# Kernel optimization log

Measured on AMD Instinct MI355X. Metric: run time of the kernel, lower is better.

The kernel has to match this reference:

```python
import jax, jax.numpy as jnp
from jax import lax
import numpy as np

D_STATE = 16
D_CONV = 4
GROUPS = 4
TOKEN = 8


def group_norm(x, w, b, groups, eps=1e-5):
    # x: [B, C, H, W]; torch GroupNorm semantics
    B, C, H, W = x.shape
    xg = x.reshape(B, groups, C // groups, H, W)
    mu = xg.mean(axis=(2, 3, 4), keepdims=True)
    var = ((xg - mu) ** 2).mean(axis=(2, 3, 4), keepdims=True)
    xg = (xg - mu) / jnp.sqrt(var + eps)
    return xg.reshape(B, C, H, W) * w[None, :, None, None] + b[None, :, None, None]


def mamba_fwd(x, in_w, conv_w, conv_b, xproj_w, dt_w, dt_b, A_log, D, out_w):
    # x: [B, L, d_model]. Faithful mamba_ssm Mamba forward (no biases on in/out proj).
    Bsz, L, _ = x.shape
    d_inner = in_w.shape[0] // 2
    dt_rank = dt_w.shape[1]
    xz = x @ in_w.T                                   # [B, L, 2*d_inner]
    xi, z = jnp.split(xz, 2, axis=-1)
    # causal depthwise conv1d (kernel D_CONV) + SiLU
    xc = lax.conv_general_dilated(
        xi.transpose(0, 2, 1), conv_w, window_strides=(1,),
        padding=[(D_CONV - 1, 0)], dimension_numbers=("NCH", "OIH", "NCH"),
        feature_group_count=d_inner)
    xc = jax.nn.silu(xc + conv_b[None, :, None]).transpose(0, 2, 1)  # [B, L, d_inner]
    xdb = xc @ xproj_w.T                               # [B, L, dt_rank + 2*d_state]
    dt, Bm, Cm = jnp.split(xdb, [dt_rank, dt_rank + D_STATE], axis=-1)
    dt = jax.nn.softplus(dt @ dt_w.T + dt_b)           # [B, L, d_inner]
    A = -jnp.exp(A_log)                                # [d_inner, d_state]
    dA = jnp.exp(dt[..., None] * A)                    # [B, L, d_inner, d_state]
    dBx = dt[..., None] * Bm[:, :, None, :] * xc[..., None]

    def step(h, inp):
        dA_t, dBx_t, C_t = inp                         # [B,di,ds],[B,di,ds],[B,ds]
        h = dA_t * h + dBx_t
        y = jnp.einsum('bds,bs->bd', h, C_t)
        return h, y

    h0 = jnp.zeros((Bsz, d_inner, D_STATE), dtype=x.dtype)
    _, ys = lax.scan(step, h0, (dA.transpose(1, 0, 2, 3),
                                dBx.transpose(1, 0, 2, 3),
                                Cm.transpose(1, 0, 2)))
    y = ys.transpose(1, 0, 2) + xc * D                 # skip term D*x
    y = y * jax.nn.silu(z)
    return y @ out_w.T


def setup_inputs() -> dict:
    key = jax.random.key(0)
    ks = iter(jax.random.split(key, 48))

    def rn(shape, s=0.02):
        return jax.random.normal(next(ks), shape, dtype=jnp.float32) * s

    B, C, H, W = 4, 64, 64, 64
    inp = {"x": jax.random.normal(next(ks), (B, C, H, W), dtype=jnp.float32)}

    def mamba_params(prefix, d_model):
        d_inner = 2 * d_model
        dt_rank = -(-d_model // 16)
        inp[prefix + "_in_w"] = rn((2 * d_inner, d_model))
        inp[prefix + "_conv_w"] = rn((d_inner, 1, D_CONV))
        inp[prefix + "_conv_b"] = rn((d_inner,))
        inp[prefix + "_xproj_w"] = rn((dt_rank + 2 * D_STATE, d_inner))
        inp[prefix + "_dt_w"] = rn((d_inner, dt_rank))
        inp[prefix + "_dt_b"] = rn((d_inner,)) + 0.5
        inp[prefix + "_A_log"] = jnp.log(jnp.tile(jnp.arange(1, D_STATE + 1, dtype=jnp.float32), (d_inner, 1)))
        inp[prefix + "_D"] = jnp.ones((d_inner,), jnp.float32)
        inp[prefix + "_out_w"] = rn((d_model, d_inner))

    mamba_params("spa", C)
    mamba_params("spe", -(-C // TOKEN))  # group_channel_num = ceil(64/8) = 8
    inp["spa_gn_w"] = jnp.ones((C,), jnp.float32)
    inp["spa_gn_b"] = jnp.zeros((C,), jnp.float32)
    inp["spe_gn_w"] = jnp.ones((C,), jnp.float32)
    inp["spe_gn_b"] = jnp.zeros((C,), jnp.float32)
    inp["att_w"] = jnp.full((2,), 0.5, jnp.float32)
    return inp


def reference(x,
              spa_in_w, spa_conv_w, spa_conv_b, spa_xproj_w, spa_dt_w, spa_dt_b,
              spa_A_log, spa_D, spa_out_w,
              spe_in_w, spe_conv_w, spe_conv_b, spe_xproj_w, spe_dt_w, spe_dt_b,
              spe_A_log, spe_D, spe_out_w,
              spa_gn_w, spa_gn_b, spe_gn_w, spe_gn_b, att_w):
    B, C, H, W = x.shape
    gcn = -(-C // TOKEN)  # C == TOKEN*gcn here, so no padding path is taken

    # --- SpaMamba: flatten all pixels into one sequence [1, B*H*W, C] ---
    xs = x.transpose(0, 2, 3, 1).reshape(1, -1, C)
    ys = mamba_fwd(xs, spa_in_w, spa_conv_w, spa_conv_b, spa_xproj_w,
                   spa_dt_w, spa_dt_b, spa_A_log, spa_D, spa_out_w)
    ys = ys.reshape(B, H, W, C).transpose(0, 3, 1, 2)
    spa = jax.nn.silu(group_norm(ys, spa_gn_w, spa_gn_b, GROUPS)) + x

    # --- SpeMamba: per-pixel spectral tokens [B*H*W, TOKEN, gcn] ---
    xe = x.transpose(0, 2, 3, 1).reshape(B * H * W, TOKEN, gcn)
    ye = mamba_fwd(xe, spe_in_w, spe_conv_w, spe_conv_b, spe_xproj_w,
                   spe_dt_w, spe_dt_b, spe_A_log, spe_D, spe_out_w)
    ye = ye.reshape(B, H, W, C).transpose(0, 3, 1, 2)
    spe = x + jax.nn.silu(group_norm(ye, spe_gn_w, spe_gn_b, GROUPS))

    w = jax.nn.softmax(att_w)
    return spa * w[0] + spe * w[1] + x
```

## Files before the change

kernel.cpp:

```cpp
#include <hip/hip_runtime.h>

__device__ __forceinline__ float siluf(float x){ return x / (1.f + __expf(-x)); }
__device__ __forceinline__ float softplusf(float x){
    return fmaxf(x, 0.f) + __logf(1.f + __expf(-fabsf(x)));
}
#if __has_builtin(__builtin_amdgcn_exp2f)
__device__ __forceinline__ float fexp2(float x){ return __builtin_amdgcn_exp2f(x); }
#else
__device__ __forceinline__ float fexp2(float x){ return exp2f(x); }
#endif

__global__ void __launch_bounds__(256) k_xpose(const float* __restrict__ x, float* __restrict__ xs){
    __shared__ float t[64][65];
    int blk = blockIdx.x;
    int b = blk >> 6;
    int hw0 = (blk & 63) << 6;
    int tid = threadIdx.x;
    if (blk == 0 && tid < 192) xs[tid] = 0.f;
    const float* xb = x + b*262144 + hw0;
    #pragma unroll
    for (int it = 0; it < 16; ++it){
        int idx = it*256 + tid;
        t[idx>>6][idx&63] = xb[(idx>>6)*4096 + (idx&63)];
    }
    __syncthreads();
    float* xsb = xs + 192 + (size_t)(b*4096 + hw0)*64;
    #pragma unroll
    for (int it = 0; it < 16; ++it){
        int idx = it*256 + tid;
        xsb[(idx>>6)*64 + (idx&63)] = t[idx&63][idx>>6];
    }
}

__global__ void __launch_bounds__(256) k_inproj_conv(const float* __restrict__ xs,
        const float* __restrict__ in_w, const float* __restrict__ cw, const float* __restrict__ cb,
        float* __restrict__ xc, float* __restrict__ zb){
    int tid = threadIdx.x;
    int l0 = blockIdx.x * 8;
    float wr[64];
    const float4* w4 = (const float4*)(in_w + tid*64);
    #pragma unroll
    for (int k = 0; k < 16; ++k){
        float4 v = w4[k];
        wr[4*k]=v.x; wr[4*k+1]=v.y; wr[4*k+2]=v.z; wr[4*k+3]=v.w;
    }
    if (tid < 128){
        float acc[11];
        #pragma unroll
        for (int r = 0; r < 11; ++r) acc[r] = 0.f;
        const float4* xr = ((const float4*)xs) + (size_t)l0*16;
        #pragma unroll
        for (int k = 0; k < 16; ++k){
            #pragma unroll
            for (int r = 0; r < 11; ++r){
                float4 v = xr[r*16 + k];
                acc[r] = fmaf(v.x, wr[4*k],   acc[r]);
                acc[r] = fmaf(v.y, wr[4*k+1], acc[r]);
                acc[r] = fmaf(v.z, wr[4*k+2], acc[r]);
                acc[r] = fmaf(v.w, wr[4*k+3], acc[r]);
            }
        }
        float cw0 = cw[tid*4+0], cw1 = cw[tid*4+1], cw2 = cw[tid*4+2], cw3 = cw[tid*4+3];
        float cbd = cb[tid];
        #pragma unroll
        for (int r = 0; r < 8; ++r){
            float a = fmaf(cw0, acc[r],   cbd);
            a = fmaf(cw1, acc[r+1], a);
            a = fmaf(cw2, acc[r+2], a);
            a = fmaf(cw3, acc[r+3], a);
            xc[(size_t)(l0+r)*128 + tid] = siluf(a);
        }
    } else {
        float acc[8];
        #pragma unroll
        for (int r = 0; r < 8; ++r) acc[r] = 0.f;
        const float4* xr = ((const float4*)(xs + 192)) + (size_t)l0*16;
        #pragma unroll
        for (int k = 0; k < 16; ++k){
            #pragma unroll
            for (int r = 0; r < 8; ++r){
                float4 v = xr[r*16 + k];
                acc[r] = fmaf(v.x, wr[4*k],   acc[r]);
                acc[r] = fmaf(v.y, wr[4*k+1], acc[r]);
                acc[r] = fmaf(v.z, wr[4*k+2], acc[r]);
                acc[r] = fmaf(v.w, wr[4*k+3], acc[r]);
            }
        }
        int dz = tid - 128;
        #pragma unroll
        for (int r = 0; r < 8; ++r) zb[(size_t)(l0+r)*128 + dz] = acc[r];
    }
}

__global__ void __launch_bounds__(256) k_scan_p1(const float* __restrict__ xc,
        const float* __restrict__ xpw, const float* __restrict__ dtw, const float* __restrict__ dtb,
        const float* __restrict__ A_log, float* __restrict__ Pb, float* __restrict__ Qb){
    __shared__ float sxc[2048];
    __shared__ float sbm[256];
    __shared__ __align__(16) float dtr[64];
    const int tid = threadIdx.x;
    const int ch = blockIdx.x;
    {
        const float4* src = (const float4*)(xc + (size_t)ch*2048);
        float4* dst = (float4*)sxc;
        dst[tid] = src[tid];
        dst[256 + tid] = src[256 + tid];
    }
    __syncthreads();
    {
        int j = tid & 63, tg = tid >> 6;
        if (j < 20){
            const float4* w4  = (const float4*)(xpw + j*128);
            const float4* xc4 = (const float4*)sxc + tg*128;
            float acc[4];
            #pragma unroll
            for (int r = 0; r < 4; ++r) acc[r] = 0.f;
            #pragma unroll 8
            for (int k = 0; k < 32; ++k){
                float4 w = w4[k];
                #pragma unroll
                for (int r = 0; r < 4; ++r){
                    float4 v = xc4[r*32 + k];
                    acc[r] = fmaf(v.x, w.x, acc[r]);
                    acc[r] = fmaf(v.y, w.y, acc[r]);
                    acc[r] = fmaf(v.z, w.z, acc[r]);
                    acc[r] = fmaf(v.w, w.w, acc[r]);
                }
            }
            if (j < 4){
                #pragma unroll
                for (int r = 0; r < 4; ++r) dtr[(tg*4+r)*4 + j] = acc[r];
            } else {
                #pragma unroll
                for (int r = 0; r < 4; ++r) sbm[(tg*4+r)*16 + (j-4)] = acc[r];
            }
        }
    }
    __syncthreads();
    const int d  = tid & 127;
    const int sh = tid >> 7;
    float A8[8];
    {
        const float4* al4 = (const float4*)(A_log + d*16 + sh*8);
        float4 v0 = al4[0], v1 = al4[1];
        A8[0]=-__expf(v0.x)*1.44269504f; A8[1]=-__expf(v0.y)*1.44269504f;
        A8[2]=-__expf(v0.z)*1.44269504f; A8[3]=-__expf(v0.w)*1.44269504f;
        A8[4]=-__expf(v1.x)*1.44269504f; A8[5]=-__expf(v1.y)*1.44269504f;
        A8[6]=-__expf(v1.z)*1.44269504f; A8[7]=-__expf(v1.w)*1.44269504f;
    }
    float4 dw = *(const float4*)(dtw + d*4);
    float dbd = dtb[d];
    float P[8], Q[8];
    #pragma unroll
    for (int s = 0; s < 8; ++s){ P[s] = 1.f; Q[s] = 0.f; }
    #pragma unroll 4
    for (int i = 0; i < 16; ++i){
        float4 dt4 = *(const float4*)(dtr + i*4);
        float dv = dbd;
        dv = fmaf(dt4.x, dw.x, dv);
        dv = fmaf(dt4.y, dw.y, dv);
        dv = fmaf(dt4.z, dw.z, dv);
        dv = fmaf(dt4.w, dw.w, dv);
        float dt = softplusf(dv);
        float db = dt * sxc[i*128 + d];
        const float4* bmr = (const float4*)(sbm + i*16 + sh*8);
        float4 b0 = bmr[0], b1 = bmr[1];
        float bv[8] = {b0.x,b0.y,b0.z,b0.w,b1.x,b1.y,b1.z,b1.w};
        #pragma unroll
        for (int s = 0; s < 8; ++s){
            float a = fexp2(dt*A8[s]);
            P[s] *= a;
            Q[s] = fmaf(a, Q[s], db*bv[s]);
        }
    }
    float* Pp = Pb + (size_t)ch*2048 + d*16 + sh*8;
    float* Qp = Qb + (size_t)ch*2048 + d*16 + sh*8;
    ((float4*)Pp)[0] = make_float4(P[0],P[1],P[2],P[3]);
    ((float4*)Pp)[1] = make_float4(P[4],P[5],P[6],P[7]);
    ((float4*)Qp)[0] = make_float4(Q[0],Q[1],Q[2],Q[3]);
    ((float4*)Qp)[1] = make_float4(Q[4],Q[5],Q[6],Q[7]);
}

#define XE_  0
#define XCL_ 1216
#define BCL_ 3904
#define DTV_ 8640
#define SPG_ 8768
__global__ void __launch_bounds__(256) k_spe(
        const float* __restrict__ x,
        const float* __restrict__ ein_w, const float* __restrict__ ecw, const float* __restrict__ ecb,
        const float* __restrict__ expw, const float* __restrict__ edtw, const float* __restrict__ edtb,
        const float* __restrict__ eA_log, const float* __restrict__ eDv, const float* __restrict__ eow,
        float* __restrict__ ye, float* __restrict__ sp)
{
    __shared__ float smem[8800];
    const int tid = threadIdx.x;
    const int pix = tid >> 4;
    const int d   = tid & 15;
    const int eb  = blockIdx.x;
    const int p0  = eb * 16;
    const int b   = p0 >> 12;
    const int hw0 = p0 & 4095;

    const float* xb = x + b*262144 + hw0;
    #pragma unroll
    for (int it = 0; it < 4; ++it){
        int idx = it*256 + tid;
        smem[XE_ + (idx&15)*76 + (idx>>4)] = xb[(idx>>4)*4096 + (idx&15)];
    }
    __syncthreads();

    float wi[8], wz[8];
    #pragma unroll
    for (int g = 0; g < 8; ++g){ wi[g] = ein_w[d*8+g]; wz[g] = ein_w[(16+d)*8+g]; }
    float xi[8], zz[8];
    {
        const float4* xe4 = (const float4*)(smem + XE_ + pix*76);
        #pragma unroll
        for (int t = 0; t < 8; ++t){
            float4 a = xe4[t*2], bq = xe4[t*2+1];
            float xv8[8] = {a.x,a.y,a.z,a.w,bq.x,bq.y,bq.z,bq.w};
            float ai = 0.f, az = 0.f;
            #pragma unroll
            for (int g = 0; g < 8; ++g){
                ai = fmaf(xv8[g], wi[g], ai);
                az = fmaf(xv8[g], wz[g], az);
            }
            xi[t] = ai; zz[t] = az;
        }
    }
    float c0 = ecw[d*4+0], c1 = ecw[d*4+1], c2 = ecw[d*4+2], c3 = ecw[d*4+3];
    float cbd = ecb[d];
    float xcr[8];
    #pragma unroll
    for (int t = 0; t < 8; ++t){
        float a = fmaf(c3, xi[t], cbd);
        if (t >= 1) a = fmaf(c2, xi[t-1], a);
        if (t >= 2) a = fmaf(c1, xi[t-2], a);
        if (t >= 3) a = fmaf(c0, xi[t-3], a);
        xcr[t] = siluf(a);
        smem[XCL_ + pix*168 + t*20 + d] = xcr[t];
    }
    __syncthreads();

    {
        const int row = tid & 127;
        const int jh  = tid >> 7;
        const int px2 = row >> 3;
        const int t2  = row & 7;
        const float4* xr = (const float4*)(smem + XCL_ + px2*168 + t2*20);
        float4 r0 = xr[0], r1 = xr[1], r2 = xr[2], r3 = xr[3];
        float xv[16] = {r0.x,r0.y,r0.z,r0.w, r1.x,r1.y,r1.z,r1.w,
                        r2.x,r2.y,r2.z,r2.w, r3.x,r3.y,r3.z,r3.w};
        const float* wbase = expw + (1 + jh*16)*16;
        float outv[16];
        #pragma unroll
        for (int s = 0; s < 16; ++s){
            const float* wr = wbase + s*16;
            float a = 0.f;
            #pragma unroll
            for (int k = 0; k < 16; ++k) a = fmaf(xv[k], wr[k], a);
            outv[s] = a;
        }
        float4* dst4 = (float4*)(smem + BCL_ + px2*296 + t2*36 + jh*16);
        dst4[0] = make_float4(outv[0], outv[1], outv[2], outv[3]);
        dst4[1] = make_float4(outv[4], outv[5], outv[6], outv[7]);
        dst4[2] = make_float4(outv[8], outv[9], outv[10],outv[11]);
        dst4[3] = make_float4(outv[12],outv[13],outv[14],outv[15]);
        if (jh == 0){
            float accd = 0.f;
            #pragma unroll
            for (int k = 0; k < 16; ++k) accd = fmaf(xv[k], expw[k], accd);
            smem[DTV_ + px2*8 + t2] = accd;
        }
    }
    __syncthreads();

    float A16[16];
    #pragma unroll
    for (int s = 0; s < 16; ++s) A16[s] = -__expf(eA_log[d*16+s]) * 1.44269504f;
    float dwd = edtw[d], dbd = edtb[d], Dd = eDv[d];
    float h[16];
    #pragma unroll
    for (int s = 0; s < 16; ++s) h[s] = 0.f;
    #pragma unroll
    for (int t = 0; t < 8; ++t){
        float dtd = softplusf(fmaf(smem[DTV_ + pix*8 + t], dwd, dbd));
        float db = dtd * xcr[t];
        const float4* bc4 = (const float4*)(smem + BCL_ + pix*296 + t*36);
        float4 b0 = bc4[0], b1 = bc4[1], b2 = bc4[2], b3 = bc4[3];
        float4 cc0 = bc4[4], cc1 = bc4[5], cc2 = bc4[6], cc3 = bc4[7];
        float bv[16] = {b0.x,b0.y,b0.z,b0.w, b1.x,b1.y,b1.z,b1.w,
                        b2.x,b2.y,b2.z,b2.w, b3.x,b3.y,b3.z,b3.w};
        float cv[16] = {cc0.x,cc0.y,cc0.z,cc0.w, cc1.x,cc1.y,cc1.z,cc1.w,
                        cc2.x,cc2.y,cc2.z,cc2.w, cc3.x,cc3.y,cc3.z,cc3.w};
        float yp = 0.f;
        #pragma unroll
        for (int s = 0; s < 16; ++s){
            float a = fexp2(dtd*A16[s]);
            h[s] = fmaf(a, h[s], db*bv[s]);
            yp = fmaf(h[s], cv[s], yp);
        }
        smem[pix*168 + t*20 + d] = (yp + xcr[t]*Dd) * siluf(zz[t]);
    }
    __syncthreads();

    {
        const int half = tid >> 7;
        const int idx7 = tid & 127;
        const int pixD = idx7 >> 3;
        const int ttD  = idx7 & 7;
        const int m0   = half*4;
        const float4* y4 = (const float4*)(smem + pixD*168 + ttD*20);
        float4 y0 = y4[0], y1 = y4[1], y2 = y4[2], y3 = y4[3];
        float ylr[16] = {y0.x,y0.y,y0.z,y0.w, y1.x,y1.y,y1.z,y1.w,
                         y2.x,y2.y,y2.z,y2.w, y3.x,y3.y,y3.z,y3.w};
        float acc[4];
        #pragma unroll
        for (int mm = 0; mm < 4; ++mm){
            const float* wr = eow + (m0+mm)*16;
            float a = 0.f;
            #pragma unroll
            for (int k = 0; k < 16; ++k) a = fmaf(ylr[k], wr[k], a);
            acc[mm] = a;
        }
        float4 o; o.x=acc[0]; o.y=acc[1]; o.z=acc[2]; o.w=acc[3];
        *(float4*)(ye + (size_t)(p0+pixD)*64 + ttD*8 + m0) = o;

        float s  = acc[0]+acc[1]+acc[2]+acc[3];
        float ss = acc[0]*acc[0]+acc[1]*acc[1]+acc[2]*acc[2]+acc[3]*acc[3];
        s += __shfl_xor(s,1);  ss += __shfl_xor(ss,1);
        s += __shfl_xor(s,8);  ss += __shfl_xor(ss,8);
        s += __shfl_xor(s,16); ss += __shfl_xor(ss,16);
        s += __shfl_xor(s,32); ss += __shfl_xor(ss,32);
        int lane = tid & 63, wv = tid >> 6;
        if ((lane & 57) == 0){
            smem[SPG_ + wv*4 + ((lane>>1)&3)] = s;
            smem[SPG_ + 16 + wv*4 + ((lane>>1)&3)] = ss;
        }
    }
    __syncthreads();
    if (tid < 4){
        int blk = eb & 255;
        float S  = smem[SPG_+0*4+tid]+smem[SPG_+1*4+tid]+smem[SPG_+2*4+tid]+smem[SPG_+3*4+tid];
        float SS = smem[SPG_+16+0*4+tid]+smem[SPG_+16+1*4+tid]+smem[SPG_+16+2*4+tid]+smem[SPG_+16+3*4+tid];
        float* dst = sp + (size_t)(((4 + b)*4 + tid)*512 + blk*2);
        dst[0] = S; dst[1] = SS;
    }
}

__global__ void __launch_bounds__(256) k_scan_p2a(const float* __restrict__ Pb,
        const float* __restrict__ Qb, float* __restrict__ Ps, float* __restrict__ Qs){
    int g = blockIdx.x*256 + threadIdx.x;
    int sup = g >> 11;
    int lane = g & 2047;
    float P = 1.f, Q = 0.f;
    for (int i = 0; i < 64; i += 8){
        float p[8], q[8];
        #pragma unroll
        for (int u = 0; u < 8; ++u){
            p[u] = Pb[(size_t)(sup*64+i+u)*2048 + lane];
            q[u] = Qb[(size_t)(sup*64+i+u)*2048 + lane];
        }
        #pragma unroll
        for (int u = 0; u < 8; ++u){
            P = p[u]*P;
            Q = fmaf(p[u], Q, q[u]);
        }
    }
    Ps[g] = P; Qs[g] = Q;
}

__global__ void __launch_bounds__(256) k_scan_p2c(const float* __restrict__ Pb,
        const float* __restrict__ Qb, const float* __restrict__ Ps,
        const float* __restrict__ Qs, float* __restrict__ Hs){
    int g = blockIdx.x*256 + threadIdx.x;
    int sup = g >> 11;
    int lane = g & 2047;
    float h = 0.f;
    for (int u = 0; u < sup; ++u){
        float p = Ps[u*2048 + lane];
        float q = Qs[u*2048 + lane];
        h = fmaf(p, h, q);
    }
    for (int i = 0; i < 64; i += 8){
        float p[8], q[8];
        #pragma unroll
        for (int u = 0; u < 8; ++u){
            p[u] = Pb[(size_t)(sup*64+i+u)*2048 + lane];
            q[u] = Qb[(size_t)(sup*64+i+u)*2048 + lane];
        }
        #pragma unroll
        for (int u = 0; u < 8; ++u){
            Hs[(size_t)(sup*64+i+u)*2048 + lane] = h;
            h = fmaf(p[u], h, q[u]);
        }
    }
}

__global__ void __launch_bounds__(256) k_scan_p3(const float* __restrict__ xc,
        const float* __restrict__ zb, const float* __restrict__ xpw, const float* __restrict__ dtw,
        const float* __restrict__ dtb, const float* __restrict__ A_log, const float* __restrict__ Dv,
        const float* __restrict__ Hs, const float* __restrict__ ow,
        float* __restrict__ ys, float* __restrict__ sp){
    __shared__ float sxc[16*128];
    __shared__ float ypl[2][16*128];
    __shared__ float sbm[16*16];
    __shared__ float scm[16*16];
    __shared__ __align__(16) float dtr[16][4];
    __shared__ float pgs[2][2][4];
    const int tid = threadIdx.x;
    const int ch = blockIdx.x;
    {
        const float4* src = (const float4*)(xc + (size_t)ch*2048);
        float4* dst = (float4*)sxc;
        dst[tid] = src[tid];
        dst[256 + tid] = src[256 + tid];
    }
    __syncthreads();
    {
        int j = tid & 63, tg = tid >> 6;
        if (j < 36){
            const float4* w4  = (const float4*)(xpw + j*128);
            const float4* xc4 = (const float4*)sxc + tg*128;
            float acc[4];
            #pragma unroll
            for (int r = 0; r < 4; ++r) acc[r] = 0.f;
            #pragma unroll 8
            for (int k = 0; k < 32; ++k){
                float4 w = w4[k];
                #pragma unroll
                for (int r = 0; r < 4; ++r){
                    float4 v = xc4[r*32 + k];
                    acc[r] = fmaf(v.x, w.x, acc[r]);
                    acc[r] = fmaf(v.y, w.y, acc[r]);
                    acc[r] = fmaf(v.z, w.z, acc[r]);
                    acc[r] = fmaf(v.w, w.w, acc[r]);
                }
            }
            if (j < 4){
                #pragma unroll
                for (int r = 0; r < 4; ++r) dtr[tg*4+r][j] = acc[r];
            } else if (j < 20){
                #pragma unroll
                for (int r = 0; r < 4; ++r) sbm[(tg*4+r)*16 + (j-4)] = acc[r];
            } else {
                #pragma unroll
                for (int r = 0; r < 4; ++r) scm[(tg*4+r)*16 + (j-20)] = acc[r];
            }
        }
    }
    __syncthreads();
    const int d  = tid & 127;
    const int sh = tid >> 7;
    float A8[8], h[8];
    {
        const float4* al4 = (const float4*)(A_log + d*16 + sh*8);
        float4 v0 = al4[0], v1 = al4[1];
        A8[0]=-__expf(v0.x)*1.44269504f; A8[1]=-__expf(v0.y)*1.44269504f;
        A8[2]=-__expf(v0.z)*1.44269504f; A8[3]=-__expf(v0.w)*1.44269504f;
        A8[4]=-__expf(v1.x)*1.44269504f; A8[5]=-__expf(v1.y)*1.44269504f;
        A8[6]=-__expf(v1.z)*1.44269504f; A8[7]=-__expf(v1.w)*1.44269504f;
        const float4* h4 = (const float4*)(Hs + (size_t)ch*2048 + d*16 + sh*8);
        float4 h0 = h4[0], h1 = h4[1];
        h[0]=h0.x; h[1]=h0.y; h[2]=h0.z; h[3]=h0.w;
        h[4]=h1.x; h[5]=h1.y; h[6]=h1.z; h[7]=h1.w;
    }
    float4 dw = *(const float4*)(dtw + d*4);
    float dbd = dtb[d];
    #pragma unroll 4
    for (int i = 0; i < 16; ++i){
        float4 dt4 = *(const float4*)dtr[i];
        float dv = dbd;
        dv = fmaf(dt4.x, dw.x, dv);
        dv = fmaf(dt4.y, dw.y, dv);
        dv = fmaf(dt4.z, dw.z, dv);
        dv = fmaf(dt4.w, dw.w, dv);
        float dt = softplusf(dv);
        float db = dt * sxc[i*128 + d];
        const float4* bmr = (const float4*)(sbm + i*16 + sh*8);
        const float4* cmr = (const float4*)(scm + i*16 + sh*8);
        float4 b0 = bmr[0], b1 = bmr[1];
        float4 c0 = cmr[0], c1 = cmr[1];
        float bv[8] = {b0.x,b0.y,b0.z,b0.w,b1.x,b1.y,b1.z,b1.w};
        float cv[8] = {c0.x,c0.y,c0.z,c0.w,c1.x,c1.y,c1.z,c1.w};
        float yp = 0.f;
        #pragma unroll
        for (int s = 0; s < 8; ++s){
            float a = fexp2(dt*A8[s]);
            h[s] = fmaf(a, h[s], db*bv[s]);
            yp = fmaf(h[s], cv[s], yp);
        }
        ypl[sh][i*128 + d] = yp;
    }
    __syncthreads();
    #pragma unroll
    for (int it = 0; it < 8; ++it){
        int idx = it*256 + tid;
        float yp = ypl[0][idx] + ypl[1][idx];
        float xcd = sxc[idx];
        float zv = zb[(size_t)ch*2048 + idx];
        ypl[0][idx] = (yp + xcd*Dv[idx & 127]) * siluf(zv);
    }
    __syncthreads();
    {
        int c  = tid & 63;
        int kh = (tid >> 6) & 1;
        int rg = tid >> 7;
        float wr[64];
        const float4* w4o = (const float4*)(ow + c*128 + kh*64);
        #pragma unroll
        for (int k = 0; k < 16; ++k){
            float4 v = w4o[k];
            wr[4*k]=v.x; wr[4*k+1]=v.y; wr[4*k+2]=v.z; wr[4*k+3]=v.w;
        }
        float acc[8];
        #pragma unroll
        for (int r = 0; r < 8; ++r) acc[r] = 0.f;
        const float4* y4 = (const float4*)(ypl[0] + rg*8*128 + kh*64);
        #pragma unroll
        for (int k = 0; k < 16; ++k){
            #pragma unroll
            for (int r = 0; r < 8; ++r){
                float4 v = y4[r*32 + k];
                acc[r] = fmaf(v.x, wr[4*k],   acc[r]);
                acc[r] = fmaf(v.y, wr[4*k+1], acc[r]);
                acc[r] = fmaf(v.z, wr[4*k+2], acc[r]);
                acc[r] = fmaf(v.w, wr[4*k+3], acc[r]);
            }
        }
        float* part = ypl[1];
        if (kh == 1){
            #pragma unroll
            for (int r = 0; r < 8; ++r) part[(rg*8+r)*64 + c] = acc[r];
        }
        __syncthreads();
        if (kh == 0){
            float s = 0.f, ss = 0.f;
            #pragma unroll
            for (int r = 0; r < 8; ++r){
                float v = acc[r] + part[(rg*8+r)*64 + c];
                ys[(size_t)(ch*16 + rg*8 + r)*64 + c] = v;
                s += v; ss += v*v;
            }
            s += __shfl_xor(s,1); ss += __shfl_xor(ss,1);
            s += __shfl_xor(s,2); ss += __shfl_xor(ss,2);
            s += __shfl_xor(s,4); ss += __shfl_xor(ss,4);
            s += __shfl_xor(s,8); ss += __shfl_xor(ss,8);
            if ((c & 15) == 0){ pgs[0][rg][c>>4] = s; pgs[1][rg][c>>4] = ss; }
        }
        __syncthreads();
        if (tid < 4){
            int b = ch >> 8, blk = ch & 255;
            float S  = pgs[0][0][tid] + pgs[0][1][tid];
            float SS = pgs[1][0][tid] + pgs[1][1][tid];
            float* dst = sp + (size_t)((b*4 + tid)*512 + blk*2);
            dst[0] = S; dst[1] = SS;
        }
    }
}

__global__ void __launch_bounds__(256) k_final(const float* __restrict__ x,
        const float* __restrict__ ys, const float* __restrict__ ye,
        const float* __restrict__ sp,
        const float* __restrict__ gsw, const float* __restrict__ gsb,
        const float* __restrict__ gew, const float* __restrict__ geb,
        const float* __restrict__ attw, float* __restrict__ out){
    __shared__ float st[16];
    __shared__ float tys[32][65];
    __shared__ float tye[32][65];
    int tid = threadIdx.x;
    int b   = blockIdx.x >> 7;
    int hw0 = (blockIdx.x & 127) << 5;
    {
        int combo = tid >> 5;
        int j = tid & 31;
        int t = combo >> 2, g = combo & 3;
        const float4* bp = (const float4*)(sp + (size_t)(t*16 + b*4 + g)*512 + j*16);
        float s = 0.f, ss = 0.f;
        #pragma unroll
        for (int k = 0; k < 4; ++k){ float4 v = bp[k]; s += v.x+v.z; ss += v.y+v.w; }
        s += __shfl_xor(s,1);  ss += __shfl_xor(ss,1);
        s += __shfl_xor(s,2);  ss += __shfl_xor(ss,2);
        s += __shfl_xor(s,4);  ss += __shfl_xor(ss,4);
        s += __shfl_xor(s,8);  ss += __shfl_xor(ss,8);
        s += __shfl_xor(s,16); ss += __shfl_xor(ss,16);
        if (j == 0){
            float m = s * (1.f/65536.f);
            float v = ss * (1.f/65536.f) - m*m;
            st[combo*2]   = m;
            st[combo*2+1] = rsqrtf(v + 1e-5f);
        }
    }
    const float* ysb = ys + ((size_t)(b*4096 + hw0))*64;
    const float* yeb = ye + ((size_t)(b*4096 + hw0))*64;
    #pragma unroll
    for (int it = 0; it < 8; ++it){
        int idx = it*256 + tid;
        tys[idx>>6][idx&63] = ysb[idx];
        tye[idx>>6][idx&63] = yeb[idx];
    }
    __syncthreads();
    float a0 = attw[0], a1 = attw[1];
    float mx = fmaxf(a0, a1);
    float e0 = __expf(a0-mx), e1 = __expf(a1-mx);
    float inv = 1.f/(e0+e1);
    float w0 = e0*inv, w1 = e1*inv;
    #pragma unroll
    for (int it = 0; it < 8; ++it){
        int idx = it*256 + tid;
        int c = idx >> 5, hwi = idx & 31;
        int g = c >> 4;
        size_t gx = ((size_t)(b*64 + c))*4096 + hw0 + hwi;
        float xv = x[gx];
        float ns = (tys[hwi][c] - st[g*2])     * st[g*2+1]     * gsw[c] + gsb[c];
        float ne = (tye[hwi][c] - st[8+g*2])   * st[8+g*2+1]   * gew[c] + geb[c];
        out[gx] = w0*(siluf(ns)+xv) + w1*(xv+siluf(ne)) + xv;
    }
}

#define OFF_XS 0u
#define OFF_XC 1048832u
#define OFF_Z  3145984u
#define OFF_PB 5243136u
#define OFF_QB 7340288u
#define OFF_HS 9437440u
#define OFF_YE 11534592u
#define OFF_PS 12583168u
#define OFF_QS 12615936u
#define OFF_SP 12648704u

extern "C" void kernel_launch(void* const* d_in, const int* in_sizes, int n_in,
                              void* d_out, int out_size, void* d_ws, size_t ws_size,
                              hipStream_t stream) {
    const float* x           = (const float*)d_in[0];
    const float* spa_in_w    = (const float*)d_in[1];
    const float* spa_conv_w  = (const float*)d_in[2];
    const float* spa_conv_b  = (const float*)d_in[3];
    const float* spa_xproj_w = (const float*)d_in[4];
    const float* spa_dt_w    = (const float*)d_in[5];
    const float* spa_dt_b    = (const float*)d_in[6];
    const float* spa_A_log   = (const float*)d_in[7];
    const float* spa_D       = (const float*)d_in[8];
    const float* spa_out_w   = (const float*)d_in[9];
    const float* spe_in_w    = (const float*)d_in[10];
    const float* spe_conv_w  = (const float*)d_in[11];
    const float* spe_conv_b  = (const float*)d_in[12];
    const float* spe_xproj_w = (const float*)d_in[13];
    const float* spe_dt_w    = (const float*)d_in[14];
    const float* spe_dt_b    = (const float*)d_in[15];
    const float* spe_A_log   = (const float*)d_in[16];
    const float* spe_D       = (const float*)d_in[17];
    const float* spe_out_w   = (const float*)d_in[18];
    const float* spa_gn_w    = (const float*)d_in[19];
    const float* spa_gn_b    = (const float*)d_in[20];
    const float* spe_gn_w    = (const float*)d_in[21];
    const float* spe_gn_b    = (const float*)d_in[22];
    const float* att_w       = (const float*)d_in[23];

    float* ws  = (float*)d_ws;
    float* xs  = ws + OFF_XS;
    float* xc  = ws + OFF_XC;
    float* zb  = ws + OFF_Z;
    float* Pb  = ws + OFF_PB;
    float* Qb  = ws + OFF_QB;
    float* Hs  = ws + OFF_HS;
    float* Ps  = ws + OFF_PS;
    float* Qs  = ws + OFF_QS;
    float* sp  = ws + OFF_SP;
    float* ysb = ws + OFF_XS;
    float* yeb = ws + OFF_YE;
    float* out = (float*)d_out;

    k_xpose      <<<256,  256, 0, stream>>>(x, xs);
    k_inproj_conv<<<2048, 256, 0, stream>>>(xs, spa_in_w, spa_conv_w, spa_conv_b, xc, zb);
    k_scan_p1    <<<1024, 256, 0, stream>>>(xc, spa_xproj_w, spa_dt_w, spa_dt_b, spa_A_log,
                                            Pb, Qb);
    k_spe        <<<1024, 256, 0, stream>>>(x, spe_in_w, spe_conv_w, spe_conv_b, spe_xproj_w,
                                            spe_dt_w, spe_dt_b, spe_A_log, spe_D, spe_out_w,
                                            yeb, sp);
    k_scan_p2a   <<<128,  256, 0, stream>>>(Pb, Qb, Ps, Qs);
    k_scan_p2c   <<<128,  256, 0, stream>>>(Pb, Qb, Ps, Qs, Hs);
    k_scan_p3    <<<1024, 256, 0, stream>>>(xc, zb, spa_xproj_w, spa_dt_w, spa_dt_b,
                                            spa_A_log, spa_D, Hs, spa_out_w, ysb, sp);
    k_final      <<<512,  256, 0, stream>>>(x, ysb, yeb, sp, spa_gn_w, spa_gn_b,
                                            spe_gn_w, spe_gn_b, att_w, out);
}
```

Baseline: 120.4 us.

## Fuse input transpose into in-proj kernel and stage spectral weights in LDS

Removes the separate transpose kernel. The in-projection/conv kernel now gathers its 11 channel-major rows (with a 3-row causal halo, zero-padded at the start) straight from x into shared memory, which saves one launch and a full write/read of the transposed buffer. The spectral kernel also preloads its small weight vectors into shared memory instead of reading them from global memory per thread. In exchange, the gathered reads from x are strided by 4096 floats per channel and so poorly coalesced, and the halo rows are loaded redundantly by neighbouring blocks.

```diff
diff --git a/kernel.cpp b/kernel.cpp
--- a/kernel.cpp
+++ b/kernel.cpp
@@ -10,33 +10,23 @@
 __device__ __forceinline__ float fexp2(float x){ return exp2f(x); }
 #endif
 
-__global__ void __launch_bounds__(256) k_xpose(const float* __restrict__ x, float* __restrict__ xs){
-    __shared__ float t[64][65];
-    int blk = blockIdx.x;
-    int b = blk >> 6;
-    int hw0 = (blk & 63) << 6;
-    int tid = threadIdx.x;
-    if (blk == 0 && tid < 192) xs[tid] = 0.f;
-    const float* xb = x + b*262144 + hw0;
-    #pragma unroll
-    for (int it = 0; it < 16; ++it){
-        int idx = it*256 + tid;
-        t[idx>>6][idx&63] = xb[(idx>>6)*4096 + (idx&63)];
-    }
-    __syncthreads();
-    float* xsb = xs + 192 + (size_t)(b*4096 + hw0)*64;
-    #pragma unroll
-    for (int it = 0; it < 16; ++it){
-        int idx = it*256 + tid;
-        xsb[(idx>>6)*64 + (idx&63)] = t[idx&63][idx>>6];
-    }
-}
-
-__global__ void __launch_bounds__(256) k_inproj_conv(const float* __restrict__ xs,
+__global__ void __launch_bounds__(256) k_inproj_conv(const float* __restrict__ x,
         const float* __restrict__ in_w, const float* __restrict__ cw, const float* __restrict__ cb,
         float* __restrict__ xc, float* __restrict__ zb){
+    __shared__ float sxe[11][68];
     int tid = threadIdx.x;
     int l0 = blockIdx.x * 8;
+    #pragma unroll
+    for (int it = 0; it < 3; ++it){
+        int idx = it*256 + tid;
+        if (idx < 704){
+            int r = idx >> 6, c = idx & 63;
+            int p = l0 - 3 + r;
+            float v = 0.f;
+            if (p >= 0) v = x[(size_t)(p >> 12)*262144 + c*4096 + (p & 4095)];
+            sxe[r][c] = v;
+        }
+    }
     float wr[64];
     const float4* w4 = (const float4*)(in_w + tid*64);
     #pragma unroll
@@ -44,16 +34,16 @@
         float4 v = w4[k];
         wr[4*k]=v.x; wr[4*k+1]=v.y; wr[4*k+2]=v.z; wr[4*k+3]=v.w;
     }
+    __syncthreads();
     if (tid < 128){
         float acc[11];
         #pragma unroll
         for (int r = 0; r < 11; ++r) acc[r] = 0.f;
-        const float4* xr = ((const float4*)xs) + (size_t)l0*16;
         #pragma unroll
         for (int k = 0; k < 16; ++k){
             #pragma unroll
             for (int r = 0; r < 11; ++r){
-                float4 v = xr[r*16 + k];
+                float4 v = *(const float4*)&sxe[r][4*k];
                 acc[r] = fmaf(v.x, wr[4*k],   acc[r]);
                 acc[r] = fmaf(v.y, wr[4*k+1], acc[r]);
                 acc[r] = fmaf(v.z, wr[4*k+2], acc[r]);
@@ -74,12 +64,11 @@
         float acc[8];
         #pragma unroll
         for (int r = 0; r < 8; ++r) acc[r] = 0.f;
-        const float4* xr = ((const float4*)(xs + 192)) + (size_t)l0*16;
         #pragma unroll
         for (int k = 0; k < 16; ++k){
             #pragma unroll
             for (int r = 0; r < 8; ++r){
-                float4 v = xr[r*16 + k];
+                float4 v = *(const float4*)&sxe[r+3][4*k];
                 acc[r] = fmaf(v.x, wr[4*k],   acc[r]);
                 acc[r] = fmaf(v.y, wr[4*k+1], acc[r]);
                 acc[r] = fmaf(v.z, wr[4*k+2], acc[r]);
@@ -181,11 +170,18 @@
     ((float4*)Qp)[1] = make_float4(Q[4],Q[5],Q[6],Q[7]);
 }
 
-#define XE_  0
-#define XCL_ 1216
-#define BCL_ 3904
-#define DTV_ 8640
-#define SPG_ 8768
+#define XE_   0
+#define XCL_  1216
+#define BCL_  3904
+#define DTV_  8640
+#define SPG_  8768
+#define WEIN_ 8800
+#define WECW_ 9056
+#define WECB_ 9120
+#define WEAL_ 9136
+#define WDTW_ 9392
+#define WDTB_ 9408
+#define WDV_  9424
 __global__ void __launch_bounds__(256) k_spe(
         const float* __restrict__ x,
         const float* __restrict__ ein_w, const float* __restrict__ ecw, const float* __restrict__ ecb,
@@ -193,7 +189,7 @@
         const float* __restrict__ eA_log, const float* __restrict__ eDv, const float* __restrict__ eow,
         float* __restrict__ ye, float* __restrict__ sp)
 {
-    __shared__ float smem[8800];
+    __shared__ float smem[9440];
     const int tid = threadIdx.x;
     const int pix = tid >> 4;
     const int d   = tid & 15;
@@ -202,6 +198,21 @@
     const int b   = p0 >> 12;
     const int hw0 = p0 & 4095;
 
+    #pragma unroll
+    for (int it = 0; it < 3; ++it){
+        int idx = it*256 + tid;
+        if (idx < 640){
+            float v;
+            if      (idx < 256) v = ein_w[idx];
+            else if (idx < 320) v = ecw[idx-256];
+            else if (idx < 336) v = ecb[idx-320];
+            else if (idx < 592) v = eA_log[idx-336];
+            else if (idx < 608) v = edtw[idx-592];
+            else if (idx < 624) v = edtb[idx-608];
+            else                v = eDv[idx-624];
+            smem[WEIN_ + idx] = v;
+        }
+    }
     const float* xb = x + b*262144 + hw0;
     #pragma unroll
     for (int it = 0; it < 4; ++it){
@@ -212,7 +223,7 @@
 
     float wi[8], wz[8];
     #pragma unroll
-    for (int g = 0; g < 8; ++g){ wi[g] = ein_w[d*8+g]; wz[g] = ein_w[(16+d)*8+g]; }
+    for (int g = 0; g < 8; ++g){ wi[g] = smem[WEIN_ + d*8+g]; wz[g] = smem[WEIN_ + 128 + d*8+g]; }
     float xi[8], zz[8];
     {
         const float4* xe4 = (const float4*)(smem + XE_ + pix*76);
@@ -229,8 +240,9 @@
             xi[t] = ai; zz[t] = az;
         }
     }
-    float c0 = ecw[d*4+0], c1 = ecw[d*4+1], c2 = ecw[d*4+2], c3 = ecw[d*4+3];
-    float cbd = ecb[d];
+    float c0 = smem[WECW_ + d*4+0], c1 = smem[WECW_ + d*4+1];
+    float c2 = smem[WECW_ + d*4+2], c3 = smem[WECW_ + d*4+3];
+    float cbd = smem[WECB_ + d];
     float xcr[8];
     #pragma unroll
     for (int t = 0; t < 8; ++t){
@@ -278,8 +290,8 @@
 
     float A16[16];
     #pragma unroll
-    for (int s = 0; s < 16; ++s) A16[s] = -__expf(eA_log[d*16+s]) * 1.44269504f;
-    float dwd = edtw[d], dbd = edtb[d], Dd = eDv[d];
+    for (int s = 0; s < 16; ++s) A16[s] = -__expf(smem[WEAL_ + d*16+s]) * 1.44269504f;
+    float dwd = smem[WDTW_ + d], dbd = smem[WDTB_ + d], Dd = smem[WDV_ + d];
     float h[16];
     #pragma unroll
     for (int s = 0; s < 16; ++s) h[s] = 0.f;
@@ -619,7 +631,7 @@
     }
 }
 
-#define OFF_XS 0u
+#define OFF_YS 0u
 #define OFF_XC 1048832u
 #define OFF_Z  3145984u
 #define OFF_PB 5243136u
@@ -659,7 +671,6 @@
     const float* att_w       = (const float*)d_in[23];
 
     float* ws  = (float*)d_ws;
-    float* xs  = ws + OFF_XS;
     float* xc  = ws + OFF_XC;
     float* zb  = ws + OFF_Z;
     float* Pb  = ws + OFF_PB;
@@ -668,12 +679,11 @@
     float* Ps  = ws + OFF_PS;
     float* Qs  = ws + OFF_QS;
     float* sp  = ws + OFF_SP;
-    float* ysb = ws + OFF_XS;
+    float* ysb = ws + OFF_YS;
     float* yeb = ws + OFF_YE;
     float* out = (float*)d_out;
 
-    k_xpose      <<<256,  256, 0, stream>>>(x, xs);
-    k_inproj_conv<<<2048, 256, 0, stream>>>(xs, spa_in_w, spa_conv_w, spa_conv_b, xc, zb);
+    k_inproj_conv<<<2048, 256, 0, stream>>>(x, spa_in_w, spa_conv_w, spa_conv_b, xc, zb);
     k_scan_p1    <<<1024, 256, 0, stream>>>(xc, spa_xproj_w, spa_dt_w, spa_dt_b, spa_A_log,
                                             Pb, Qb);
     k_spe        <<<1024, 256, 0, stream>>>(x, spe_in_w, spe_conv_w, spe_conv_b, spe_xproj_w,
```

New measurement: 118.4 us (median of 2 runs). Within noise of the previous version (-1.7%).
